# Kernel tuning notes

Measured on AMD Instinct MI355X. Metric: run time of the kernel, lower is better.

## Reference

```python
import jax, jax.numpy as jnp
import numpy as np

B, N, D, H = 4, 2048, 1024, 16
DK = D // H
LAMBDA = 0.5


def _linear_params(key, fan_in, fan_out):
    kw, kb = jax.random.split(key)
    bound = 1.0 / np.sqrt(fan_in)
    W = jax.random.uniform(kw, (fan_in, fan_out), jnp.float32, -bound, bound)
    b = jax.random.uniform(kb, (fan_out,), jnp.float32, -bound, bound)
    return W, b


def setup_inputs() -> dict:
    key = jax.random.key(0)
    ks = jax.random.split(key, 10)
    x = jax.random.normal(ks[0], (B, N, D), jnp.float32)
    # binary DAG-like adjacency (sparse-ish)
    causal_graph = jax.random.bernoulli(ks[1], 0.05, (N, N)).astype(jnp.float32)
    # differentiable backdoor mask: exp(-lambda*|Z|), 0 where no valid backdoor set
    Z = jax.random.randint(ks[2], (N, N), 0, 6).astype(jnp.float32)
    exists = jax.random.bernoulli(ks[3], 0.8, (N, N)).astype(jnp.float32)
    backdoor_mask = jnp.exp(-LAMBDA * Z) * exists
    Wq, bq = _linear_params(ks[4], D, D)
    Wk, bk = _linear_params(ks[5], D, D)
    Wc, bc = _linear_params(ks[6], N, D)  # W_cause: n_variables -> d_model
    We, be = _linear_params(ks[7], N, D)  # W_effect: n_variables -> d_model
    Wv, bv = _linear_params(ks[8], D, D)
    Wo, bo = _linear_params(ks[9], D, D)
    return dict(x=x, causal_graph=causal_graph, backdoor_mask=backdoor_mask,
                Wq=Wq, bq=bq, Wk=Wk, bk=bk, Wc=Wc, bc=bc, We=We, be=be,
                Wv=Wv, bv=bv, Wo=Wo, bo=bo)


def reference(x, causal_graph, backdoor_mask, Wq, bq, Wk, bk, Wc, bc, We, be, Wv, bv, Wo, bo):
    # Formula 5: asymmetric causal Q/K projections
    Q = x @ Wq + bq + (causal_graph @ Wc + bc)[None]        # [B,N,D]
    K = x @ Wk + bk + (causal_graph.T @ We + be)[None]      # [B,N,D]
    V = x @ Wv + bv                                          # [B,N,D]
    Qh = Q.reshape(B, N, H, DK)
    Kh = K.reshape(B, N, H, DK)
    Vh = V.reshape(B, N, H, DK)
    scores = jnp.einsum('bihd,bjhd->bhij', Qh, Kh) / np.sqrt(DK).astype(np.float32)
    # backdoor mask is MULTIPLICATIVE on raw scores (pre-softmax)
    scores = scores * backdoor_mask[None, None]
    attn = jax.nn.softmax(scores, axis=-1)                  # [B,H,N,N]
    out = jnp.einsum('bhij,bjhd->bihd', attn, Vh).reshape(B, N, D)
    return out @ Wo + bo
```

## Files before the change

kernel.cpp:

```cpp
#include <hip/hip_runtime.h>
#include <hip/hip_bf16.h>

#define BB 4
#define NN 2048
#define DD 1024
#define HH 16

using bf16 = __hip_bfloat16;
typedef __attribute__((ext_vector_type(8))) short bf16x8s;
typedef __attribute__((ext_vector_type(4))) float f32x4;

#define GLOAD_LDS16(gp, lp)                                                   \
  __builtin_amdgcn_global_load_lds(                                           \
      (const __attribute__((address_space(1))) void*)(gp),                    \
      (__attribute__((address_space(3))) void*)(lp), 16, 0, 0)

__global__ void cast_f32_bf16(const float* __restrict__ in, bf16* __restrict__ out, int n) {
  int i = (blockIdx.x * blockDim.x + threadIdx.x) * 4;
  if (i >= n) return;
  float4 v = *reinterpret_cast<const float4*>(in + i);
  ushort4 o;
  bf16 t0 = __float2bfloat16(v.x); o.x = *reinterpret_cast<unsigned short*>(&t0);
  bf16 t1 = __float2bfloat16(v.y); o.y = *reinterpret_cast<unsigned short*>(&t1);
  bf16 t2 = __float2bfloat16(v.z); o.z = *reinterpret_cast<unsigned short*>(&t2);
  bf16 t3 = __float2bfloat16(v.w); o.w = *reinterpret_cast<unsigned short*>(&t3);
  *reinterpret_cast<ushort4*>(out + i) = o;
}

__global__ void transpose_cast(const float* __restrict__ in, bf16* __restrict__ out, int R, int C) {
  __shared__ float t[32][33];
  int c0 = blockIdx.x * 32, r0 = blockIdx.y * 32;
  int tx = threadIdx.x, ty = threadIdx.y;
#pragma unroll
  for (int i = 0; i < 4; i++)
    t[ty + i * 8][tx] = in[(size_t)(r0 + ty + i * 8) * C + c0 + tx];
  __syncthreads();
#pragma unroll
  for (int i = 0; i < 4; i++)
    out[(size_t)(c0 + ty + i * 8) * R + r0 + tx] = __float2bfloat16(t[tx][ty + i * 8]);
}

__global__ void transpose_v(const bf16* __restrict__ Vb, bf16* __restrict__ Vt) {
  __shared__ short t[32][33];
  int bh = blockIdx.z; int b = bh >> 4, h = bh & 15;
  int n0 = blockIdx.x * 32, d0 = blockIdx.y * 32;
  int tx = threadIdx.x, ty = threadIdx.y;
#pragma unroll
  for (int i = 0; i < 4; i++)
    t[ty + i * 8][tx] = reinterpret_cast<const short*>(Vb)[
        (size_t)(b * NN + n0 + ty + i * 8) * DD + h * 64 + d0 + tx];
  __syncthreads();
#pragma unroll
  for (int i = 0; i < 4; i++)
    reinterpret_cast<short*>(Vt)[(size_t)(bh * 64 + d0 + ty + i * 8) * NN + n0 + tx] =
        t[tx][ty + i * 8];
}

template <int OUT_BF16, int HAS_ROWADD>
__device__ __forceinline__ void gemm_tile(
    const bf16* __restrict__ A, const bf16* __restrict__ BT, void* __restrict__ Cout,
    const float* __restrict__ bias, const float* __restrict__ rowadd,
    int Nc, int K, float scale, int brow, int bcol, short* As, short* Bs) {
  const int tid = threadIdx.x;
  const int l = tid & 63, w = tid >> 6;
  const int wr = (w >> 1) * 64, wc = (w & 1) * 64;
  const int lr = l & 15, lg = l >> 4;
  const int swz = lr & 7;
  f32x4 acc[4][4] = {};
  for (int k0 = 0; k0 < K; k0 += 64) {
#pragma unroll
    for (int i = 0; i < 4; i++) {
      int c = i * 256 + tid;
      int row = c >> 3, gch = (c & 7) ^ (row & 7);
      short* lA = As + (size_t)(i * 256 + w * 64) * 8;
      GLOAD_LDS16(A + (size_t)(brow + row) * K + k0 + gch * 8, lA);
      short* lB = Bs + (size_t)(i * 256 + w * 64) * 8;
      GLOAD_LDS16(BT + (size_t)(bcol + row) * K + k0 + gch * 8, lB);
    }
    __syncthreads();
#pragma unroll
    for (int t = 0; t < 2; t++) {
      bf16x8s a[4], bfr[4];
#pragma unroll
      for (int m = 0; m < 4; m++)
        a[m] = *reinterpret_cast<const bf16x8s*>(
            &As[(wr + m * 16 + lr) * 64 + ((t * 4 + lg) ^ swz) * 8]);
#pragma unroll
      for (int n = 0; n < 4; n++)
        bfr[n] = *reinterpret_cast<const bf16x8s*>(
            &Bs[(wc + n * 16 + lr) * 64 + ((t * 4 + lg) ^ swz) * 8]);
#pragma unroll
      for (int m = 0; m < 4; m++)
#pragma unroll
        for (int n = 0; n < 4; n++)
          acc[m][n] = __builtin_amdgcn_mfma_f32_16x16x32_bf16(a[m], bfr[n], acc[m][n], 0, 0, 0);
    }
    __syncthreads();
  }
#pragma unroll
  for (int m = 0; m < 4; m++) {
#pragma unroll
    for (int n = 0; n < 4; n++) {
      int col = bcol + wc + n * 16 + lr;
      float bv = bias[col];
#pragma unroll
      for (int r = 0; r < 4; r++) {
        int row = brow + wr + m * 16 + lg * 4 + r;
        float v = acc[m][n][r] + bv;
        if (HAS_ROWADD) v += rowadd[(size_t)(row & (NN - 1)) * Nc + col];
        v *= scale;
        if (OUT_BF16)
          reinterpret_cast<bf16*>(Cout)[(size_t)row * Nc + col] = __float2bfloat16(v);
        else
          reinterpret_cast<float*>(Cout)[(size_t)row * Nc + col] = v;
      }
    }
  }
}

template <int OUT_BF16, int HAS_ROWADD>
__global__ __launch_bounds__(256) void gemm_bt(
    const bf16* __restrict__ A, const bf16* __restrict__ BT, void* __restrict__ Cout,
    const float* __restrict__ bias, const float* __restrict__ rowadd,
    int M, int Nc, int K, float scale) {
  __shared__ short As[128 * 64];
  __shared__ short Bs[128 * 64];
  const int nbx = gridDim.x;
  const int nwg = nbx * gridDim.y;
  const int wg = blockIdx.y * nbx + blockIdx.x;
  const int swg = (wg & 7) * (nwg >> 3) + (wg >> 3);
  const int bxi = swg % nbx, byi = swg / nbx;
  gemm_tile<OUT_BF16, HAS_ROWADD>(A, BT, Cout, bias, rowadd, Nc, K, scale,
                                  byi * 128, bxi * 128, As, Bs);
}

__global__ __launch_bounds__(256) void gemm_dual(
    const bf16* __restrict__ A0, const bf16* __restrict__ B0, float* __restrict__ C0,
    const float* __restrict__ bias0,
    const bf16* __restrict__ A1, const bf16* __restrict__ B1, float* __restrict__ C1,
    const float* __restrict__ bias1, int Nc, int K) {
  __shared__ short As[128 * 64];
  __shared__ short Bs[128 * 64];
  const int nbx = gridDim.x;
  const int nwg = nbx * gridDim.y;
  const int wg = blockIdx.y * nbx + blockIdx.x;
  const int swg = (wg & 7) * (nwg >> 3) + (wg >> 3);
  const int bxi = swg % nbx, byi = swg / nbx;
  if (blockIdx.z == 0)
    gemm_tile<0, 0>(A0, B0, C0, bias0, nullptr, Nc, K, 1.0f, byi * 128, bxi * 128, As, Bs);
  else
    gemm_tile<0, 0>(A1, B1, C1, bias1, nullptr, Nc, K, 1.0f, byi * 128, bxi * 128, As, Bs);
}

__global__ __launch_bounds__(256) void attn_k(
    const bf16* __restrict__ Qb, const bf16* __restrict__ Kb, const bf16* __restrict__ Vt,
    const float* __restrict__ mask, bf16* __restrict__ Ob) {
  constexpr int PPAD = 72;
  __shared__ short Ks[64 * 64];
  __shared__ short Vts[64 * 64];
  __shared__ short Ps[4][16 * PPAD];
  const int tid = threadIdx.x;
  const int wg = blockIdx.x;
  const int x = wg & 7, i = wg >> 3;
  const int b = x >> 1;
  const int h = ((x & 1) << 3) | (i & 7);
  const int q0 = ((i >> 3) & 31) * 64;
  const int l = tid & 63, w = tid >> 6;
  const int lr = l & 15, lg = l >> 4, lk = lg * 8;
  const int swz = lr & 7;

  const size_t qoff = (size_t)(b * NN + q0 + w * 16 + lr) * DD + h * 64;
  bf16x8s qf0 = *reinterpret_cast<const bf16x8s*>(Qb + qoff + lk);
  bf16x8s qf1 = *reinterpret_cast<const bf16x8s*>(Qb + qoff + 32 + lk);

  f32x4 acc[4] = {};
  float mrun = -1e30f, lrun = 0.f;

  const size_t kbase = (size_t)b * NN * DD + h * 64;
  const size_t vbase = (size_t)(b * HH + h) * 64 * NN;
  const float* mptr = mask + (size_t)(q0 + w * 16 + lr) * NN + lg * 4;

  const int r0 = tid >> 3, ch0 = tid & 7;
  const int r1 = 32 + (tid >> 3);
  const bf16* kg0 = Kb + kbase + (size_t)r0 * DD + ch0 * 8;
  const bf16* kg1 = Kb + kbase + (size_t)r1 * DD + ch0 * 8;
  const bf16* vg0 = Vt + vbase + (size_t)r0 * NN + ch0 * 8;
  const bf16* vg1 = Vt + vbase + (size_t)r1 * NN + ch0 * 8;
  short* kw0 = &Ks[r0 * 64 + (ch0 ^ (r0 & 7)) * 8];
  short* kw1 = &Ks[r1 * 64 + (ch0 ^ (r1 & 7)) * 8];
  short* vw0 = &Vts[r0 * 64 + (ch0 ^ (r0 & 7)) * 8];
  short* vw1 = &Vts[r1 * 64 + (ch0 ^ (r1 & 7)) * 8];

  uint4 kr0, kr1, vr0, vr1;
  float4 m0, m1, m2, m3;
  float4 n0, n1, n2, n3;
  kr0 = *reinterpret_cast<const uint4*>(kg0);
  kr1 = *reinterpret_cast<const uint4*>(kg1);
  vr0 = *reinterpret_cast<const uint4*>(vg0);
  vr1 = *reinterpret_cast<const uint4*>(vg1);
  m0 = *reinterpret_cast<const float4*>(mptr + 0);
  m1 = *reinterpret_cast<const float4*>(mptr + 16);
  m2 = *reinterpret_cast<const float4*>(mptr + 32);
  m3 = *reinterpret_cast<const float4*>(mptr + 48);

  for (int jt = 0; jt < NN; jt += 64) {
    __syncthreads();
    *reinterpret_cast<uint4*>(kw0) = kr0;
    *reinterpret_cast<uint4*>(kw1) = kr1;
    *reinterpret_cast<uint4*>(vw0) = vr0;
    *reinterpret_cast<uint4*>(vw1) = vr1;
    if (jt + 64 < NN) {
      kr0 = *reinterpret_cast<const uint4*>(kg0 + (size_t)(jt + 64) * DD);
      kr1 = *reinterpret_cast<const uint4*>(kg1 + (size_t)(jt + 64) * DD);
      vr0 = *reinterpret_cast<const uint4*>(vg0 + jt + 64);
      vr1 = *reinterpret_cast<const uint4*>(vg1 + jt + 64);
      n0 = *reinterpret_cast<const float4*>(mptr + jt + 64 + 0);
      n1 = *reinterpret_cast<const float4*>(mptr + jt + 64 + 16);
      n2 = *reinterpret_cast<const float4*>(mptr + jt + 64 + 32);
      n3 = *reinterpret_cast<const float4*>(mptr + jt + 64 + 48);
    }
    __syncthreads();

    f32x4 s[4];
#pragma unroll
    for (int jj = 0; jj < 4; jj++) {
      bf16x8s k0 = *reinterpret_cast<const bf16x8s*>(
          &Ks[(jj * 16 + lr) * 64 + ((0 + lg) ^ swz) * 8]);
      bf16x8s k1 = *reinterpret_cast<const bf16x8s*>(
          &Ks[(jj * 16 + lr) * 64 + ((4 + lg) ^ swz) * 8]);
      f32x4 z = {0.f, 0.f, 0.f, 0.f};
      z = __builtin_amdgcn_mfma_f32_16x16x32_bf16(k0, qf0, z, 0, 0, 0);
      s[jj] = __builtin_amdgcn_mfma_f32_16x16x32_bf16(k1, qf1, z, 0, 0, 0);
    }

    float lv[4][4];
    lv[0][0] = s[0][0] * m0.x; lv[0][1] = s[0][1] * m0.y;
    lv[0][2] = s[0][2] * m0.z; lv[0][3] = s[0][3] * m0.w;
    lv[1][0] = s[1][0] * m1.x; lv[1][1] = s[1][1] * m1.y;
    lv[1][2] = s[1][2] * m1.z; lv[1][3] = s[1][3] * m1.w;
    lv[2][0] = s[2][0] * m2.x; lv[2][1] = s[2][1] * m2.y;
    lv[2][2] = s[2][2] * m2.z; lv[2][3] = s[2][3] * m2.w;
    lv[3][0] = s[3][0] * m3.x; lv[3][1] = s[3][1] * m3.y;
    lv[3][2] = s[3][2] * m3.z; lv[3][3] = s[3][3] * m3.w;
    m0 = n0; m1 = n1; m2 = n2; m3 = n3;

    float mx0 = fmaxf(fmaxf(lv[0][0], lv[0][1]), fmaxf(lv[0][2], lv[0][3]));
    float mx1 = fmaxf(fmaxf(lv[1][0], lv[1][1]), fmaxf(lv[1][2], lv[1][3]));
    float mx2 = fmaxf(fmaxf(lv[2][0], lv[2][1]), fmaxf(lv[2][2], lv[2][3]));
    float mx3 = fmaxf(fmaxf(lv[3][0], lv[3][1]), fmaxf(lv[3][2], lv[3][3]));
    float mx = fmaxf(fmaxf(mx0, mx1), fmaxf(mx2, mx3));
    mx = fmaxf(mx, __shfl_xor(mx, 16, 64));
    mx = fmaxf(mx, __shfl_xor(mx, 32, 64));

    if (__any(mx > mrun + 11.0f)) {
      float mnew = fmaxf(mrun, mx);
      float sc = __builtin_amdgcn_exp2f(mrun - mnew);
      mrun = mnew;
      lrun *= sc;
#pragma unroll
      for (int s4 = 0; s4 < 4; s4++)
#pragma unroll
        for (int r = 0; r < 4; r++) acc[s4][r] *= sc;
    }

    short* Pw = &Ps[w][0];
    float rs = 0.f;
#pragma unroll
    for (int jj = 0; jj < 4; jj++) {
      float p0 = __builtin_amdgcn_exp2f(lv[jj][0] - mrun);
      float p1 = __builtin_amdgcn_exp2f(lv[jj][1] - mrun);
      float p2 = __builtin_amdgcn_exp2f(lv[jj][2] - mrun);
      float p3 = __builtin_amdgcn_exp2f(lv[jj][3] - mrun);
      rs += (p0 + p1) + (p2 + p3);
      ushort4 pk;
      bf16 b0 = __float2bfloat16(p0); pk.x = *reinterpret_cast<unsigned short*>(&b0);
      bf16 b1 = __float2bfloat16(p1); pk.y = *reinterpret_cast<unsigned short*>(&b1);
      bf16 b2 = __float2bfloat16(p2); pk.z = *reinterpret_cast<unsigned short*>(&b2);
      bf16 b3 = __float2bfloat16(p3); pk.w = *reinterpret_cast<unsigned short*>(&b3);
      *reinterpret_cast<ushort4*>(&Pw[lr * PPAD + jj * 16 + lg * 4]) = pk;
    }
    rs += __shfl_xor(rs, 16, 64);
    rs += __shfl_xor(rs, 32, 64);
    lrun += rs;

    asm volatile("s_waitcnt lgkmcnt(0)" ::: "memory");
    __builtin_amdgcn_sched_barrier(0);

    bf16x8s pb0 = *reinterpret_cast<const bf16x8s*>(&Pw[lr * PPAD + lk]);
    bf16x8s pb1 = *reinterpret_cast<const bf16x8s*>(&Pw[lr * PPAD + 32 + lk]);
#pragma unroll
    for (int s4 = 0; s4 < 4; s4++) {
      bf16x8s v0 = *reinterpret_cast<const bf16x8s*>(
          &Vts[(s4 * 16 + lr) * 64 + ((0 + lg) ^ swz) * 8]);
      bf16x8s v1 = *reinterpret_cast<const bf16x8s*>(
          &Vts[(s4 * 16 + lr) * 64 + ((4 + lg) ^ swz) * 8]);
      acc[s4] = __builtin_amdgcn_mfma_f32_16x16x32_bf16(v0, pb0, acc[s4], 0, 0, 0);
      acc[s4] = __builtin_amdgcn_mfma_f32_16x16x32_bf16(v1, pb1, acc[s4], 0, 0, 0);
    }
  }

  float rl = __builtin_amdgcn_rcpf(lrun);
  const size_t orow = (size_t)(b * NN + q0 + w * 16 + lr) * DD + h * 64;
#pragma unroll
  for (int s4 = 0; s4 < 4; s4++) {
    ushort4 o;
    bf16 b0 = __float2bfloat16(acc[s4][0] * rl); o.x = *reinterpret_cast<unsigned short*>(&b0);
    bf16 b1 = __float2bfloat16(acc[s4][1] * rl); o.y = *reinterpret_cast<unsigned short*>(&b1);
    bf16 b2 = __float2bfloat16(acc[s4][2] * rl); o.z = *reinterpret_cast<unsigned short*>(&b2);
    bf16 b3 = __float2bfloat16(acc[s4][3] * rl); o.w = *reinterpret_cast<unsigned short*>(&b3);
    *reinterpret_cast<ushort4*>(reinterpret_cast<unsigned short*>(Ob) + orow + s4 * 16 + lg * 4) = o;
  }
}

extern "C" void kernel_launch(void* const* d_in, const int* in_sizes, int n_in,
                              void* d_out, int out_size, void* d_ws, size_t ws_size,
                              hipStream_t stream) {
  (void)in_sizes; (void)n_in; (void)out_size; (void)ws_size;
  const float* x    = (const float*)d_in[0];
  const float* cg   = (const float*)d_in[1];
  const float* mask = (const float*)d_in[2];
  const float* Wq   = (const float*)d_in[3];
  const float* bq   = (const float*)d_in[4];
  const float* Wk   = (const float*)d_in[5];
  const float* bk   = (const float*)d_in[6];
  const float* Wc   = (const float*)d_in[7];
  const float* bc   = (const float*)d_in[8];
  const float* We   = (const float*)d_in[9];
  const float* be   = (const float*)d_in[10];
  const float* Wv   = (const float*)d_in[11];
  const float* bv   = (const float*)d_in[12];
  const float* Wo   = (const float*)d_in[13];
  const float* bo   = (const float*)d_in[14];

  auto MB = [](size_t m) { return m << 20; };
  char* ws = (char*)d_ws;
  bf16* xb   = (bf16*)(ws + MB(0));
  bf16* WqT  = (bf16*)(ws + MB(16));
  bf16* WkT  = (bf16*)(ws + MB(18));
  bf16* WvT  = (bf16*)(ws + MB(20));
  bf16* WoT  = (bf16*)(ws + MB(22));
  float* cq  = (float*)(ws + MB(24));
  float* ck  = (float*)(ws + MB(32));
  bf16* Qb   = (bf16*)(ws + MB(40));
  bf16* Kb   = (bf16*)(ws + MB(56));
  bf16* Vb   = (bf16*)(ws + MB(72));
  bf16* Vt   = (bf16*)(ws + MB(88));
  bf16* Ob   = (bf16*)(ws + MB(72));
  bf16* WcT  = (bf16*)(ws + MB(40));
  bf16* WeT  = (bf16*)(ws + MB(44));
  bf16* cgb  = (bf16*)(ws + MB(48));
  bf16* cgT  = (bf16*)(ws + MB(56));

  cast_f32_bf16<<<dim3(BB * NN * DD / 4 / 256), 256, 0, stream>>>(x, xb, BB * NN * DD);
  cast_f32_bf16<<<dim3(NN * NN / 4 / 256), 256, 0, stream>>>(cg, cgb, NN * NN);
  dim3 tb(32, 8);
  transpose_cast<<<dim3(DD / 32, DD / 32), tb, 0, stream>>>(Wq, WqT, DD, DD);
  transpose_cast<<<dim3(DD / 32, DD / 32), tb, 0, stream>>>(Wk, WkT, DD, DD);
  transpose_cast<<<dim3(DD / 32, DD / 32), tb, 0, stream>>>(Wv, WvT, DD, DD);
  transpose_cast<<<dim3(DD / 32, DD / 32), tb, 0, stream>>>(Wo, WoT, DD, DD);
  transpose_cast<<<dim3(DD / 32, NN / 32), tb, 0, stream>>>(Wc, WcT, NN, DD);
  transpose_cast<<<dim3(DD / 32, NN / 32), tb, 0, stream>>>(We, WeT, NN, DD);
  transpose_cast<<<dim3(NN / 32, NN / 32), tb, 0, stream>>>(cg, cgT, NN, NN);

  gemm_dual<<<dim3(DD / 128, NN / 128, 2), 256, 0, stream>>>(
      cgb, WcT, cq, bc, cgT, WeT, ck, be, DD, NN);
  gemm_bt<1, 1><<<dim3(DD / 128, BB * NN / 128), 256, 0, stream>>>(
      xb, WqT, Qb, bq, cq, BB * NN, DD, DD, 0.125f * 1.4426950408889634f);
  gemm_bt<1, 1><<<dim3(DD / 128, BB * NN / 128), 256, 0, stream>>>(xb, WkT, Kb, bk, ck, BB * NN, DD, DD, 1.0f);
  gemm_bt<1, 0><<<dim3(DD / 128, BB * NN / 128), 256, 0, stream>>>(xb, WvT, Vb, bv, nullptr, BB * NN, DD, DD, 1.0f);

  transpose_v<<<dim3(NN / 32, 2, BB * HH), tb, 0, stream>>>(Vb, Vt);

  attn_k<<<dim3(NN / 64 * HH * BB), 256, 0, stream>>>(Qb, Kb, Vt, mask, Ob);

  gemm_bt<0, 0><<<dim3(DD / 128, BB * NN / 128), 256, 0, stream>>>(Ob, WoT, (float*)d_out, bo, nullptr, BB * NN, DD, DD, 1.0f);
}
```

Baseline: 348.1 us.

## Use 128-query attention tiles with 512 threads and batch weight transposes

The attention kernel now runs 8 waves per block over a 128-row query tile, so each K/V tile staged in LDS is reused by twice as many query rows. Each thread now loads a single K and V chunk instead of two. The mask is loaded inside the loop rather than register-prefetched a tile ahead, which lowers register pressure but exposes that load latency. The four DxD weight transpose launches are merged into one launch indexed by blockIdx.z, cutting launch overhead.

Result: faster. 315.8 us (-9.3%).

```diff
diff --git a/kernel.cpp b/kernel.cpp
--- a/kernel.cpp
+++ b/kernel.cpp
@@ -27,7 +27,8 @@
   *reinterpret_cast<ushort4*>(out + i) = o;
 }
 
-__global__ void transpose_cast(const float* __restrict__ in, bf16* __restrict__ out, int R, int C) {
+__device__ __forceinline__ void transpose_tile(const float* __restrict__ in,
+                                               bf16* __restrict__ out, int R, int C) {
   __shared__ float t[32][33];
   int c0 = blockIdx.x * 32, r0 = blockIdx.y * 32;
   int tx = threadIdx.x, ty = threadIdx.y;
@@ -38,6 +39,24 @@
 #pragma unroll
   for (int i = 0; i < 4; i++)
     out[(size_t)(c0 + ty + i * 8) * R + r0 + tx] = __float2bfloat16(t[tx][ty + i * 8]);
+}
+
+__global__ void transpose_cast(const float* __restrict__ in, bf16* __restrict__ out, int R, int C) {
+  transpose_tile(in, out, R, C);
+}
+
+__global__ void transpose_cast4(const float* __restrict__ W0, const float* __restrict__ W1,
+                                const float* __restrict__ W2, const float* __restrict__ W3,
+                                bf16* __restrict__ O0, bf16* __restrict__ O1,
+                                bf16* __restrict__ O2, bf16* __restrict__ O3) {
+  const float* in; bf16* out;
+  switch (blockIdx.z) {
+    case 0: in = W0; out = O0; break;
+    case 1: in = W1; out = O1; break;
+    case 2: in = W2; out = O2; break;
+    default: in = W3; out = O3; break;
+  }
+  transpose_tile(in, out, DD, DD);
 }
 
 __global__ void transpose_v(const bf16* __restrict__ Vb, bf16* __restrict__ Vt) {
@@ -152,19 +171,19 @@
     gemm_tile<0, 0>(A1, B1, C1, bias1, nullptr, Nc, K, 1.0f, byi * 128, bxi * 128, As, Bs);
 }
 
-__global__ __launch_bounds__(256) void attn_k(
+__global__ __launch_bounds__(512, 4) void attn_k(
     const bf16* __restrict__ Qb, const bf16* __restrict__ Kb, const bf16* __restrict__ Vt,
     const float* __restrict__ mask, bf16* __restrict__ Ob) {
   constexpr int PPAD = 72;
   __shared__ short Ks[64 * 64];
   __shared__ short Vts[64 * 64];
-  __shared__ short Ps[4][16 * PPAD];
+  __shared__ short Ps[8][16 * PPAD];
   const int tid = threadIdx.x;
   const int wg = blockIdx.x;
   const int x = wg & 7, i = wg >> 3;
   const int b = x >> 1;
   const int h = ((x & 1) << 3) | (i & 7);
-  const int q0 = ((i >> 3) & 31) * 64;
+  const int q0 = ((i >> 3) & 15) * 128;
   const int l = tid & 63, w = tid >> 6;
   const int lr = l & 15, lg = l >> 4, lk = lg * 8;
   const int swz = lr & 7;
@@ -181,43 +200,26 @@
   const float* mptr = mask + (size_t)(q0 + w * 16 + lr) * NN + lg * 4;
 
   const int r0 = tid >> 3, ch0 = tid & 7;
-  const int r1 = 32 + (tid >> 3);
   const bf16* kg0 = Kb + kbase + (size_t)r0 * DD + ch0 * 8;
-  const bf16* kg1 = Kb + kbase + (size_t)r1 * DD + ch0 * 8;
   const bf16* vg0 = Vt + vbase + (size_t)r0 * NN + ch0 * 8;
-  const bf16* vg1 = Vt + vbase + (size_t)r1 * NN + ch0 * 8;
   short* kw0 = &Ks[r0 * 64 + (ch0 ^ (r0 & 7)) * 8];
-  short* kw1 = &Ks[r1 * 64 + (ch0 ^ (r1 & 7)) * 8];
   short* vw0 = &Vts[r0 * 64 + (ch0 ^ (r0 & 7)) * 8];
-  short* vw1 = &Vts[r1 * 64 + (ch0 ^ (r1 & 7)) * 8];
-
-  uint4 kr0, kr1, vr0, vr1;
-  float4 m0, m1, m2, m3;
-  float4 n0, n1, n2, n3;
+
+  uint4 kr0, vr0;
   kr0 = *reinterpret_cast<const uint4*>(kg0);
-  kr1 = *reinterpret_cast<const uint4*>(kg1);
   vr0 = *reinterpret_cast<const uint4*>(vg0);
-  vr1 = *reinterpret_cast<const uint4*>(vg1);
-  m0 = *reinterpret_cast<const float4*>(mptr + 0);
-  m1 = *reinterpret_cast<const float4*>(mptr + 16);
-  m2 = *reinterpret_cast<const float4*>(mptr + 32);
-  m3 = *reinterpret_cast<const float4*>(mptr + 48);
 
   for (int jt = 0; jt < NN; jt += 64) {
     __syncthreads();
     *reinterpret_cast<uint4*>(kw0) = kr0;
-    *reinterpret_cast<uint4*>(kw1) = kr1;
     *reinterpret_cast<uint4*>(vw0) = vr0;
-    *reinterpret_cast<uint4*>(vw1) = vr1;
+    float4 m0 = *reinterpret_cast<const float4*>(mptr + jt + 0);
+    float4 m1 = *reinterpret_cast<const float4*>(mptr + jt + 16);
+    float4 m2 = *reinterpret_cast<const float4*>(mptr + jt + 32);
+    float4 m3 = *reinterpret_cast<const float4*>(mptr + jt + 48);
     if (jt + 64 < NN) {
       kr0 = *reinterpret_cast<const uint4*>(kg0 + (size_t)(jt + 64) * DD);
-      kr1 = *reinterpret_cast<const uint4*>(kg1 + (size_t)(jt + 64) * DD);
       vr0 = *reinterpret_cast<const uint4*>(vg0 + jt + 64);
-      vr1 = *reinterpret_cast<const uint4*>(vg1 + jt + 64);
-      n0 = *reinterpret_cast<const float4*>(mptr + jt + 64 + 0);
-      n1 = *reinterpret_cast<const float4*>(mptr + jt + 64 + 16);
-      n2 = *reinterpret_cast<const float4*>(mptr + jt + 64 + 32);
-      n3 = *reinterpret_cast<const float4*>(mptr + jt + 64 + 48);
     }
     __syncthreads();
 
@@ -242,7 +244,6 @@
     lv[2][2] = s[2][2] * m2.z; lv[2][3] = s[2][3] * m2.w;
     lv[3][0] = s[3][0] * m3.x; lv[3][1] = s[3][1] * m3.y;
     lv[3][2] = s[3][2] * m3.z; lv[3][3] = s[3][3] * m3.w;
-    m0 = n0; m1 = n1; m2 = n2; m3 = n3;
 
     float mx0 = fmaxf(fmaxf(lv[0][0], lv[0][1]), fmaxf(lv[0][2], lv[0][3]));
     float mx1 = fmaxf(fmaxf(lv[1][0], lv[1][1]), fmaxf(lv[1][2], lv[1][3]));
@@ -354,10 +355,8 @@
   cast_f32_bf16<<<dim3(BB * NN * DD / 4 / 256), 256, 0, stream>>>(x, xb, BB * NN * DD);
   cast_f32_bf16<<<dim3(NN * NN / 4 / 256), 256, 0, stream>>>(cg, cgb, NN * NN);
   dim3 tb(32, 8);
-  transpose_cast<<<dim3(DD / 32, DD / 32), tb, 0, stream>>>(Wq, WqT, DD, DD);
-  transpose_cast<<<dim3(DD / 32, DD / 32), tb, 0, stream>>>(Wk, WkT, DD, DD);
-  transpose_cast<<<dim3(DD / 32, DD / 32), tb, 0, stream>>>(Wv, WvT, DD, DD);
-  transpose_cast<<<dim3(DD / 32, DD / 32), tb, 0, stream>>>(Wo, WoT, DD, DD);
+  transpose_cast4<<<dim3(DD / 32, DD / 32, 4), tb, 0, stream>>>(
+      Wq, Wk, Wv, Wo, WqT, WkT, WvT, WoT);
   transpose_cast<<<dim3(DD / 32, NN / 32), tb, 0, stream>>>(Wc, WcT, NN, DD);
   transpose_cast<<<dim3(DD / 32, NN / 32), tb, 0, stream>>>(We, WeT, NN, DD);
   transpose_cast<<<dim3(NN / 32, NN / 32), tb, 0, stream>>>(cg, cgT, NN, NN);
@@ -366,12 +365,15 @@
       cgb, WcT, cq, bc, cgT, WeT, ck, be, DD, NN);
   gemm_bt<1, 1><<<dim3(DD / 128, BB * NN / 128), 256, 0, stream>>>(
       xb, WqT, Qb, bq, cq, BB * NN, DD, DD, 0.125f * 1.4426950408889634f);
-  gemm_bt<1, 1><<<dim3(DD / 128, BB * NN / 128), 256, 0, stream>>>(xb, WkT, Kb, bk, ck, BB * NN, DD, DD, 1.0f);
-  gemm_bt<1, 0><<<dim3(DD / 128, BB * NN / 128), 256, 0, stream>>>(xb, WvT, Vb, bv, nullptr, BB * NN, DD, DD, 1.0f);
+  gemm_bt<1, 1><<<dim3(DD / 128, BB * NN / 128), 256, 0, stream>>>(
+      xb, WkT, Kb, bk, ck, BB * NN, DD, DD, 1.0f);
+  gemm_bt<1, 0><<<dim3(DD / 128, BB * NN / 128), 256, 0, stream>>>(
+      xb, WvT, Vb, bv, nullptr, BB * NN, DD, DD, 1.0f);
 
   transpose_v<<<dim3(NN / 32, 2, BB * HH), tb, 0, stream>>>(Vb, Vt);
 
-  attn_k<<<dim3(NN / 64 * HH * BB), 256, 0, stream>>>(Qb, Kb, Vt, mask, Ob);
-
-  gemm_bt<0, 0><<<dim3(DD / 128, BB * NN / 128), 256, 0, stream>>>(Ob, WoT, (float*)d_out, bo, nullptr, BB * NN, DD, DD, 1.0f);
-}
+  attn_k<<<dim3(NN / 128 * HH * BB), 512, 0, stream>>>(Qb, Kb, Vt, mask, Ob);
+
+  gemm_bt<0, 0><<<dim3(DD / 128, BB * NN / 128), 256, 0, stream>>>(
+      Ob, WoT, (float*)d_out, bo, nullptr, BB * NN, DD, DD, 1.0f);
+}
```
